# Performance work log

Hardware: AMD Instinct MI355X
Metric: run time of the kernel (lower is better)

Reference implementation:

```python
import jax, jax.numpy as jnp
import numpy as np

WIN = 7            # skimage default win_size
NP_ = WIN * WIN    # pixels per 2D window (per channel)
COV_NORM = NP_ / (NP_ - 1.0)  # use_sample_covariance=True
K1, K2 = 0.01, 0.03


def setup_inputs() -> dict:
    key = jax.random.key(0)
    k1, k2 = jax.random.split(key)
    img1 = jax.random.uniform(k1, (32, 3, 512, 512), dtype=jnp.float32)
    img2 = jax.random.uniform(k2, (32, 3, 512, 512), dtype=jnp.float32)
    return {"img1": img1, "img2": img2}


def _uf(x):
    # valid 7x7 uniform (mean) filter; x: [N, 1, H, W] -> [N, 1, H-6, W-6]
    # independent of boundary mode.
    k = jnp.ones((1, 1, WIN, WIN), x.dtype) / NP_
    return jax.lax.conv_general_dilated(
        x, k, window_strides=(1, 1), padding='VALID',
        dimension_numbers=('NCHW', 'OIHW', 'NCHW'))


def reference(img1, img2):
    B, C, H, W = img1.shape
    x = img1.reshape(B * C, 1, H, W)
    y = img2.reshape(B * C, 1, H, W)

    ux, uy = _uf(x), _uf(y)
    uxx, uyy, uxy = _uf(x * x), _uf(y * y), _uf(x * y)
    vx = COV_NORM * (uxx - ux * ux)
    vy = COV_NORM * (uyy - uy * uy)
    vxy = COV_NORM * (uxy - ux * uy)

    # per-image data_range = img2[i].max() - img2[i].min() (over C,H,W)
    dr = jnp.max(img2, axis=(1, 2, 3)) - jnp.min(img2, axis=(1, 2, 3))  # [B]
    dr = jnp.repeat(dr, C).reshape(B * C, 1, 1, 1)
    C1 = (K1 * dr) ** 2
    C2 = (K2 * dr) ** 2

    S = ((2.0 * ux * uy + C1) * (2.0 * vxy + C2)) / \
        ((ux * ux + uy * uy + C1) * (vx + vy + C2))

    # skimage: mean over cropped map per channel, mean over channels, then batch mean
    ssim_per_img = S.reshape(B, C, H - WIN + 1, W - WIN + 1).mean(axis=(1, 2, 3))
    return 1.0 - ssim_per_img.mean()
```

## Files before the change

kernel.cpp:

```cpp
#include <hip/hip_runtime.h>

#define IMG_H 512
#define IMG_W 512
#define NIMG 96
#define WOUT 506
#define STRIP 11
#define NSTRIPS 46
#define NBLK (NSTRIPS*NIMG)
#define TOTAL_VALS 24579456.0f

__device__ __forceinline__ unsigned fkey(float f){
    unsigned b = __float_as_uint(f);
    return (b & 0x80000000u) ? ~b : (b | 0x80000000u);
}
__device__ __forceinline__ float fdec(unsigned k){
    unsigned b = (k & 0x80000000u) ? (k ^ 0x80000000u) : ~k;
    return __uint_as_float(b);
}

__global__ __launch_bounds__(256) void minmax_kernel(const float4* __restrict__ y4,
                                                     unsigned* __restrict__ maxk,
                                                     unsigned* __restrict__ mink){
    int blk  = blockIdx.x;
    int img  = blk >> 6;
    int chnk = blk & 63;
    const float4* base = y4 + (size_t)img * 196608 + (size_t)chnk * 3072;
    float mn = 3.4e38f, mx = -3.4e38f;
    for (int i = threadIdx.x; i < 3072; i += 256){
        float4 v = base[i];
        mn = fminf(mn, fminf(fminf(v.x, v.y), fminf(v.z, v.w)));
        mx = fmaxf(mx, fmaxf(fmaxf(v.x, v.y), fmaxf(v.z, v.w)));
    }
    #pragma unroll
    for (int off = 32; off; off >>= 1){
        mn = fminf(mn, __shfl_down(mn, off));
        mx = fmaxf(mx, __shfl_down(mx, off));
    }
    if ((threadIdx.x & 63) == 0){
        atomicMax(&maxk[img], fkey(mx));
        atomicMin(&mink[img], fkey(mn));
    }
}


#define ROWOP(row, OPA) { \
    const float* xr = x + (size_t)(row)*IMG_W + c0; \
    const float* yr = y + (size_t)(row)*IMG_W + c0; \
    float4 xa = *(const float4*)xr;     float4 xb = *(const float4*)(xr+4); \
    float4 ya = *(const float4*)yr;     float4 yb = *(const float4*)(yr+4); \
    float xv[8] = {xa.x,xa.y,xa.z,xa.w,xb.x,xb.y,xb.z,xb.w}; \
    float yv[8] = {ya.x,ya.y,ya.z,ya.w,yb.x,yb.y,yb.z,yb.w}; \
    _Pragma("unroll") \
    for (int k = 0; k < 8; k++){ \
        sx[k]  OPA xv[k]; \
        sy[k]  OPA yv[k]; \
        sxx[k] OPA xv[k]*xv[k]; \
        syy[k] OPA yv[k]*yv[k]; \
        sxy[k] OPA xv[k]*yv[k]; \
    } }

#define HSHUF(s, outw) { \
    float n0=__shfl_down(s[0],1), n1=__shfl_down(s[1],1), n2=__shfl_down(s[2],1); \
    float n3=__shfl_down(s[3],1), n4=__shfl_down(s[4],1), n5=__shfl_down(s[5],1); \
    float w = s[0]+s[1]+s[2]+s[3]+s[4]+s[5]+s[6]; \
    outw[0]=w; \
    w += s[7]-s[0]; outw[1]=w; \
    w += n0-s[1];   outw[2]=w; \
    w += n1-s[2];   outw[3]=w; \
    w += n2-s[3];   outw[4]=w; \
    w += n3-s[4];   outw[5]=w; \
    w += n4-s[5];   outw[6]=w; \
    w += n5-s[6];   outw[7]=w; }

__global__ __launch_bounds__(64) void ssim_kernel(const float* __restrict__ img1,
                                                  const float* __restrict__ img2,
                                                  const unsigned* __restrict__ maxk,
                                                  const unsigned* __restrict__ mink,
                                                  float* __restrict__ acc){
    int bid = blockIdx.x;
    int L   = (bid & 7) * (NBLK/8) + (bid >> 3);
    int img   = L / NSTRIPS;
    int strip = L - img * NSTRIPS;
    int b     = img / 3;

    float dr = fdec(maxk[b]) - fdec(mink[b]);
    float c1 = 0.01f * dr;  c1 *= c1;
    float c2 = 0.03f * dr;  c2 *= c2;
    const float c1s = 2401.0f * c1;
    const float c2s = 2401.0f * c2;
    const float CO2 = 2.0f * 49.0f / 48.0f;
    const float COV = 49.0f / 48.0f;

    const float* x = img1 + (size_t)img * (IMG_H*IMG_W);
    const float* y = img2 + (size_t)img * (IMG_H*IMG_W);

    int t  = threadIdx.x;
    int c0 = t * 8;

    float sx[8]={0,0,0,0,0,0,0,0}, sy[8]={0,0,0,0,0,0,0,0};
    float sxx[8]={0,0,0,0,0,0,0,0}, syy[8]={0,0,0,0,0,0,0,0}, sxy[8]={0,0,0,0,0,0,0,0};

    int r0 = strip * STRIP;

    for (int rr = 0; rr < 7; rr++){ ROWOP(r0+rr, +=) }

    float accS = 0.0f;

    for (int r = r0; r < r0 + STRIP; r++){
        float wsx[8], wsy[8], wsxx[8], wsyy[8], wsxy[8];
        HSHUF(sx, wsx)  HSHUF(sy, wsy)  HSHUF(sxx, wsxx)
        HSHUF(syy, wsyy)  HSHUF(sxy, wsxy)

        #pragma unroll
        for (int j = 0; j < 8; j++){
            if (c0 + j < WOUT){
                float P = wsx[j], Q = wsy[j];
                float t1 = P*Q;
                float t2 = fmaf(P, P, Q*Q);
                float a1 = fmaf(2.0f, t1, c1s);
                float b1 = t2 + c1s;
                float u  = fmaf(49.0f, wsxy[j], -t1);
                float a2 = fmaf(CO2, u, c2s);
                float v  = fmaf(49.0f, wsxx[j]+wsyy[j], -t2);
                float b2 = fmaf(COV, v, c2s);
                accS += (a1*a2) * __builtin_amdgcn_rcpf(b1*b2);
            }
        }

        if (r < r0 + STRIP - 1){
            ROWOP(r+7, +=)
            ROWOP(r,   -=)
        }
    }

    #pragma unroll
    for (int off = 32; off; off >>= 1)
        accS += __shfl_down(accS, off);
    if (t == 0)
        atomicAdd(acc, accS);
}

__global__ void finalize_kernel(const float* __restrict__ acc, float* __restrict__ out){
    out[0] = 1.0f - acc[0] * (1.0f / TOTAL_VALS);
}

extern "C" void kernel_launch(void* const* d_in, const int* in_sizes, int n_in,
                              void* d_out, int out_size, void* d_ws, size_t ws_size,
                              hipStream_t stream) {
    const float* img1 = (const float*)d_in[0];
    const float* img2 = (const float*)d_in[1];
    float* out = (float*)d_out;

    char* ws = (char*)d_ws;
    float*    acc  = (float*)ws;
    unsigned* maxk = (unsigned*)(ws + 128);
    unsigned* mink = (unsigned*)(ws + 256);

    hipMemsetAsync(ws, 0, 256, stream);
    hipMemsetAsync(ws + 256, 0xFF, 128, stream);

    minmax_kernel<<<2048, 256, 0, stream>>>((const float4*)img2, maxk, mink);
    ssim_kernel<<<NBLK, 64, 0, stream>>>(img1, img2, maxk, mink, acc);
    finalize_kernel<<<1, 1, 0, stream>>>(acc, out);
}
```

Baseline: 356.5 us.

## Replace atomic min/max and sum with per-strip partials and prefetch rows

Per-image min/max is now computed per strip into workspace slots, using the same block swizzle as the SSIM kernel. Each SSIM block reduces the 138 partials for its image, writes its own strip sum, and a final kernel reduces those sums. This removes the memset launches and the global atomics. The SSIM row loop also issues the loads for the next entering and leaving rows before the shuffle and compute phase, so memory latency overlaps with arithmetic. In exchange, each SSIM block does a redundant serial 138-element reduction, the min/max pass reads overlapping rows, and an atomic fallback path is kept for small workspaces.

```diff
diff --git a/kernel.cpp b/kernel.cpp
--- a/kernel.cpp
+++ b/kernel.cpp
@@ -9,25 +9,27 @@
 #define NBLK (NSTRIPS*NIMG)
 #define TOTAL_VALS 24579456.0f
 
-__device__ __forceinline__ unsigned fkey(float f){
-    unsigned b = __float_as_uint(f);
-    return (b & 0x80000000u) ? ~b : (b | 0x80000000u);
-}
-__device__ __forceinline__ float fdec(unsigned k){
-    unsigned b = (k & 0x80000000u) ? (k ^ 0x80000000u) : ~k;
-    return __uint_as_float(b);
-}
-
-__global__ __launch_bounds__(256) void minmax_kernel(const float4* __restrict__ y4,
-                                                     unsigned* __restrict__ maxk,
-                                                     unsigned* __restrict__ mink){
-    int blk  = blockIdx.x;
-    int img  = blk >> 6;
-    int chnk = blk & 63;
-    const float4* base = y4 + (size_t)img * 196608 + (size_t)chnk * 3072;
+#define WS_MN 0
+#define WS_MX 8192
+#define WS_SS 16384
+#define WS_NEED ((WS_SS + NBLK) * 4)
+
+__device__ __forceinline__ int swz(int bid){
+    return (bid & 7) * (NBLK / 8) + (bid >> 3);
+}
+
+__global__ __launch_bounds__(64) void minmax_part(const float* __restrict__ img2,
+                                                  float* __restrict__ ws){
+    int L     = swz(blockIdx.x);
+    int img   = L / NSTRIPS;
+    int strip = L - img * NSTRIPS;
+    int r0    = strip * STRIP;
+
+    const float4* y4 = (const float4*)(img2 + (size_t)img * (IMG_H*IMG_W)) + r0 * 128;
     float mn = 3.4e38f, mx = -3.4e38f;
-    for (int i = threadIdx.x; i < 3072; i += 256){
-        float4 v = base[i];
+    #pragma unroll 4
+    for (int i = threadIdx.x; i < 17*128; i += 64){
+        float4 v = y4[i];
         mn = fminf(mn, fminf(fminf(v.x, v.y), fminf(v.z, v.w)));
         mx = fmaxf(mx, fmaxf(fmaxf(v.x, v.y), fmaxf(v.z, v.w)));
     }
@@ -36,9 +38,9 @@
         mn = fminf(mn, __shfl_down(mn, off));
         mx = fmaxf(mx, __shfl_down(mx, off));
     }
-    if ((threadIdx.x & 63) == 0){
-        atomicMax(&maxk[img], fkey(mx));
-        atomicMin(&mink[img], fkey(mn));
+    if (threadIdx.x == 0){
+        ws[WS_MN + L] = mn;
+        ws[WS_MX + L] = mx;
     }
 }
 
@@ -72,18 +74,33 @@
     w += n4-s[5];   outw[6]=w; \
     w += n5-s[6];   outw[7]=w; }
 
+template<int USE_WS>
 __global__ __launch_bounds__(64) void ssim_kernel(const float* __restrict__ img1,
                                                   const float* __restrict__ img2,
-                                                  const unsigned* __restrict__ maxk,
-                                                  const unsigned* __restrict__ mink,
+                                                  float* __restrict__ ws,
                                                   float* __restrict__ acc){
-    int bid = blockIdx.x;
-    int L   = (bid & 7) * (NBLK/8) + (bid >> 3);
+    int L     = swz(blockIdx.x);
     int img   = L / NSTRIPS;
     int strip = L - img * NSTRIPS;
     int b     = img / 3;
 
-    float dr = fdec(maxk[b]) - fdec(mink[b]);
+    float mn = 3.4e38f, mx = -3.4e38f;
+    if (USE_WS){
+        const float* pmn = ws + WS_MN + b * 3 * NSTRIPS;
+        const float* pmx = ws + WS_MX + b * 3 * NSTRIPS;
+        #pragma unroll 6
+        for (int i = 0; i < 3*NSTRIPS; i++){
+            mn = fminf(mn, pmn[i]);
+            mx = fmaxf(mx, pmx[i]);
+        }
+    } else {
+        unsigned mk = ((const unsigned*)ws)[b];
+        unsigned nk = ((const unsigned*)ws)[32 + b];
+        unsigned mb = (mk & 0x80000000u) ? (mk ^ 0x80000000u) : ~mk;
+        unsigned nb = (nk & 0x80000000u) ? (nk ^ 0x80000000u) : ~nk;
+        mx = __uint_as_float(mb); mn = __uint_as_float(nb);
+    }
+    float dr = mx - mn;
     float c1 = 0.01f * dr;  c1 *= c1;
     float c2 = 0.03f * dr;  c2 *= c2;
     const float c1s = 2401.0f * c1;
@@ -102,11 +119,25 @@
 
     int r0 = strip * STRIP;
 
+    #pragma unroll
     for (int rr = 0; rr < 7; rr++){ ROWOP(r0+rr, +=) }
 
     float accS = 0.0f;
 
     for (int r = r0; r < r0 + STRIP; r++){
+        bool more = (r < r0 + STRIP - 1);
+        float4 EX0,EX1,EY0,EY1, LX0,LX1,LY0,LY1;
+        if (more){
+            const float* xe = x + (size_t)(r+7)*IMG_W + c0;
+            const float* ye = y + (size_t)(r+7)*IMG_W + c0;
+            const float* xl = x + (size_t)r*IMG_W + c0;
+            const float* yl = y + (size_t)r*IMG_W + c0;
+            EX0 = *(const float4*)xe;  EX1 = *(const float4*)(xe+4);
+            EY0 = *(const float4*)ye;  EY1 = *(const float4*)(ye+4);
+            LX0 = *(const float4*)xl;  LX1 = *(const float4*)(xl+4);
+            LY0 = *(const float4*)yl;  LY1 = *(const float4*)(yl+4);
+        }
+
         float wsx[8], wsy[8], wsxx[8], wsyy[8], wsxy[8];
         HSHUF(sx, wsx)  HSHUF(sy, wsy)  HSHUF(sxx, wsxx)
         HSHUF(syy, wsyy)  HSHUF(sxy, wsxy)
@@ -127,21 +158,69 @@
             }
         }
 
-        if (r < r0 + STRIP - 1){
-            ROWOP(r+7, +=)
-            ROWOP(r,   -=)
+        if (more){
+            float xv[8] = {EX0.x,EX0.y,EX0.z,EX0.w,EX1.x,EX1.y,EX1.z,EX1.w};
+            float yv[8] = {EY0.x,EY0.y,EY0.z,EY0.w,EY1.x,EY1.y,EY1.z,EY1.w};
+            float lx[8] = {LX0.x,LX0.y,LX0.z,LX0.w,LX1.x,LX1.y,LX1.z,LX1.w};
+            float ly[8] = {LY0.x,LY0.y,LY0.z,LY0.w,LY1.x,LY1.y,LY1.z,LY1.w};
+            #pragma unroll
+            for (int k = 0; k < 8; k++){
+                sx[k]  += xv[k] - lx[k];
+                sy[k]  += yv[k] - ly[k];
+                sxx[k] += xv[k]*xv[k] - lx[k]*lx[k];
+                syy[k] += yv[k]*yv[k] - ly[k]*ly[k];
+                sxy[k] += xv[k]*yv[k] - lx[k]*ly[k];
+            }
         }
     }
 
     #pragma unroll
     for (int off = 32; off; off >>= 1)
         accS += __shfl_down(accS, off);
-    if (t == 0)
-        atomicAdd(acc, accS);
-}
-
-__global__ void finalize_kernel(const float* __restrict__ acc, float* __restrict__ out){
+    if (t == 0){
+        if (USE_WS) ws[WS_SS + L] = accS;
+        else        atomicAdd(acc, accS);
+    }
+}
+
+__global__ __launch_bounds__(64) void finalize_ws(const float* __restrict__ ws,
+                                                  float* __restrict__ out){
+    float s = 0.0f;
+    for (int i = threadIdx.x; i < NBLK; i += 64) s += ws[WS_SS + i];
+    #pragma unroll
+    for (int off = 32; off; off >>= 1) s += __shfl_down(s, off);
+    if (threadIdx.x == 0) out[0] = 1.0f - s * (1.0f / TOTAL_VALS);
+}
+
+__global__ void finalize_acc(const float* __restrict__ acc, float* __restrict__ out){
     out[0] = 1.0f - acc[0] * (1.0f / TOTAL_VALS);
+}
+
+__device__ __forceinline__ unsigned fkey(float f){
+    unsigned b = __float_as_uint(f);
+    return (b & 0x80000000u) ? ~b : (b | 0x80000000u);
+}
+__global__ __launch_bounds__(256) void minmax_atomic(const float4* __restrict__ y4,
+                                                     unsigned* __restrict__ ws){
+    int blk  = blockIdx.x;
+    int img  = blk >> 6;
+    int chnk = blk & 63;
+    const float4* base = y4 + (size_t)img * 196608 + (size_t)chnk * 3072;
+    float mn = 3.4e38f, mx = -3.4e38f;
+    for (int i = threadIdx.x; i < 3072; i += 256){
+        float4 v = base[i];
+        mn = fminf(mn, fminf(fminf(v.x, v.y), fminf(v.z, v.w)));
+        mx = fmaxf(mx, fmaxf(fmaxf(v.x, v.y), fmaxf(v.z, v.w)));
+    }
+    #pragma unroll
+    for (int off = 32; off; off >>= 1){
+        mn = fminf(mn, __shfl_down(mn, off));
+        mx = fmaxf(mx, __shfl_down(mx, off));
+    }
+    if ((threadIdx.x & 63) == 0){
+        atomicMax(&ws[img], fkey(mx));
+        atomicMin(&ws[32 + img], fkey(mn));
+    }
 }
 
 extern "C" void kernel_launch(void* const* d_in, const int* in_sizes, int n_in,
@@ -150,16 +229,19 @@
     const float* img1 = (const float*)d_in[0];
     const float* img2 = (const float*)d_in[1];
     float* out = (float*)d_out;
-
-    char* ws = (char*)d_ws;
-    float*    acc  = (float*)ws;
-    unsigned* maxk = (unsigned*)(ws + 128);
-    unsigned* mink = (unsigned*)(ws + 256);
-
-    hipMemsetAsync(ws, 0, 256, stream);
-    hipMemsetAsync(ws + 256, 0xFF, 128, stream);
-
-    minmax_kernel<<<2048, 256, 0, stream>>>((const float4*)img2, maxk, mink);
-    ssim_kernel<<<NBLK, 64, 0, stream>>>(img1, img2, maxk, mink, acc);
-    finalize_kernel<<<1, 1, 0, stream>>>(acc, out);
-}
+    float* ws  = (float*)d_ws;
+
+    if (ws_size >= WS_NEED){
+        minmax_part<<<NBLK, 64, 0, stream>>>(img2, ws);
+        ssim_kernel<1><<<NBLK, 64, 0, stream>>>(img1, img2, ws, nullptr);
+        finalize_ws<<<1, 64, 0, stream>>>(ws, out);
+    } else {
+        hipMemsetAsync(ws, 0, 160, stream);
+        hipMemsetAsync((char*)ws + 128, 0xFF, 128, stream);
+        hipMemsetAsync((char*)ws + 256, 0, 16, stream);
+        float* acc = ws + 64;
+        minmax_atomic<<<2048, 256, 0, stream>>>((const float4*)img2, (unsigned*)ws);
+        ssim_kernel<0><<<NBLK, 64, 0, stream>>>(img1, img2, ws, acc);
+        finalize_acc<<<1, 1, 0, stream>>>(acc, out);
+    }
+}
```

Result: faster. 287.5 us (-19.4%).
